# Kernel optimization log

Hardware: AMD Instinct MI355X
Metric: run time of the kernel (lower is better)

The kernel has to match this reference:

```python
import jax, jax.numpy as jnp
import numpy as np

DIM = 512
NUM_HEADS = 4  # min(4, 512 // 16)
HEAD_DIM = DIM // NUM_HEADS  # 128


def setup_inputs() -> dict:
    key = jax.random.key(0)
    ks = jax.random.split(key, 5)
    B, N = 2, 4096
    s = DIM ** -0.5
    return {
        "x": jax.random.normal(ks[0], (B, N, DIM), dtype=jnp.float32),
        "qkv_w": jax.random.normal(ks[1], (3 * DIM, DIM), dtype=jnp.float32) * s,
        "qkv_b": jax.random.normal(ks[2], (3 * DIM,), dtype=jnp.float32) * 0.02,
        "proj_w": jax.random.normal(ks[3], (DIM, DIM), dtype=jnp.float32) * s,
        "proj_b": jax.random.normal(ks[4], (DIM,), dtype=jnp.float32) * 0.02,
    }


def reference(x, qkv_w, qkv_b, proj_w, proj_b):
    B, N, C = x.shape
    H, D = NUM_HEADS, HEAD_DIM
    # torch Linear: x @ W^T + b
    qkv = x @ qkv_w.T + qkv_b                      # [B, N, 3C]
    qkv = qkv.reshape(B, N, 3, H, D)
    q = qkv[:, :, 0].transpose(0, 2, 1, 3)         # [B, H, N, D]
    k = qkv[:, :, 1].transpose(0, 2, 1, 3)
    v = qkv[:, :, 2].transpose(0, 2, 1, 3)
    scale = D ** -0.5
    attn = jnp.einsum('bhnd,bhmd->bhnm', q, k) * scale  # [B, H, N, N]
    attn = jax.nn.softmax(attn, axis=-1)
    # dropout(p=0.1) is identity in eval mode
    out = jnp.einsum('bhnm,bhmd->bhnd', attn, v)   # [B, H, N, D]
    out = out.transpose(0, 2, 1, 3).reshape(B, N, C)
    return out @ proj_w.T + proj_b
```

## Files before the change

### kernel.cpp

```cpp
#include <hip/hip_runtime.h>
#include <hip/hip_bf16.h>
#include <stdint.h>

constexpr int B_  = 2;
constexpr int N_  = 4096;
constexpr int C_  = 512;
constexpr int H_  = 4;
constexpr int D_  = 128;
constexpr int M_  = B_ * N_;
constexpr int TC_ = 3 * C_;
constexpr float SCALE_  = 0.08838834764831845f;
constexpr float LOG2E_  = 1.4426950408889634f;
constexpr float KSCALE_ = SCALE_ * LOG2E_;

typedef __attribute__((ext_vector_type(8))) short short8;
typedef __attribute__((ext_vector_type(4))) float f32x4;

#define GLOBAL_AS __attribute__((address_space(1)))
#define LDS_AS    __attribute__((address_space(3)))

static __device__ __forceinline__ void load_lds16(const void* gp, void* lp) {
    __builtin_amdgcn_global_load_lds((const GLOBAL_AS void*)gp, (LDS_AS void*)lp,
                                     16, 0, 0);
}

static __device__ __forceinline__ uint16_t f2bf(float f) {
    uint32_t u = __builtin_bit_cast(uint32_t, f);
    uint32_t r = (u + 0x7FFFu + ((u >> 16) & 1u)) >> 16;
    return (uint16_t)r;
}
static __device__ __forceinline__ uint32_t cvt_pk_bf16(float lo, float hi) {
    uint32_t r;
    asm("v_cvt_pk_bf16_f32 %0, %1, %2" : "=v"(r) : "v"(lo), "v"(hi));
    return r;
}
static __device__ __forceinline__ float exp2f_fast(float x) {
    float r;
    asm("v_exp_f32 %0, %1" : "=v"(r) : "v"(x));
    return r;
}

__global__ __launch_bounds__(256)
void cast_kernel(const float* __restrict__ src, uint16_t* __restrict__ dst, int n8)
{
    for (int i = blockIdx.x * blockDim.x + threadIdx.x; i < n8;
         i += gridDim.x * blockDim.x) {
        float4 a = reinterpret_cast<const float4*>(src)[2*i];
        float4 b = reinterpret_cast<const float4*>(src)[2*i+1];
        uint4 o;
        o.x = (uint32_t)f2bf(a.x) | ((uint32_t)f2bf(a.y) << 16);
        o.y = (uint32_t)f2bf(a.z) | ((uint32_t)f2bf(a.w) << 16);
        o.z = (uint32_t)f2bf(b.x) | ((uint32_t)f2bf(b.y) << 16);
        o.w = (uint32_t)f2bf(b.z) | ((uint32_t)f2bf(b.w) << 16);
        reinterpret_cast<uint4*>(dst)[i] = o;
    }
}

__global__ __launch_bounds__(256, 2)
void gemm_qkv(const uint16_t* __restrict__ A,
              const uint16_t* __restrict__ Bw,
              const float* __restrict__ bias,
              uint16_t* __restrict__ Qb,
              uint16_t* __restrict__ Kb,
              uint16_t* __restrict__ Vt)
{
    __shared__ __align__(16) uint16_t As[128 * 64];
    __shared__ __align__(16) uint16_t Bs[128 * 64];

    const int tid  = threadIdx.x;
    const int lane = tid & 63;
    const int w    = tid >> 6;
    const int wr   = w >> 1, wc = w & 1;
    const int cq   = lane & 15;
    const int g    = lane >> 4;
    const int m0   = blockIdx.x * 128;
    const int o0   = blockIdx.y * 128;

    f32x4 acc[4][4];
    const f32x4 zf = {0.f, 0.f, 0.f, 0.f};
    #pragma unroll
    for (int i = 0; i < 4; ++i)
        #pragma unroll
        for (int j = 0; j < 4; ++j) acc[i][j] = zf;

    for (int kt = 0; kt < C_; kt += 64) {
        __syncthreads();
        #pragma unroll
        for (int i = 0; i < 4; ++i) {
            int s = tid + 256 * i;
            int row = s >> 3, p = s & 7, c = p ^ (row & 7);
            load_lds16(A  + (size_t)(m0 + row) * C_ + kt + c * 8, &As[row*64 + p*8]);
            load_lds16(Bw + (size_t)(o0 + row) * C_ + kt + c * 8, &Bs[row*64 + p*8]);
        }
        __syncthreads();
        #pragma unroll
        for (int ks = 0; ks < 2; ++ks) {
            short8 af[4], bfr[4];
            #pragma unroll
            for (int mi = 0; mi < 4; ++mi) {
                int r = 64*wr + 16*mi + cq;
                af[mi] = *reinterpret_cast<const short8*>(
                    &As[r*64 + (((g + 4*ks) ^ (r & 7)) * 8)]);
            }
            #pragma unroll
            for (int ni = 0; ni < 4; ++ni) {
                int r = 64*wc + 16*ni + cq;
                bfr[ni] = *reinterpret_cast<const short8*>(
                    &Bs[r*64 + (((g + 4*ks) ^ (r & 7)) * 8)]);
            }
            #pragma unroll
            for (int mi = 0; mi < 4; ++mi)
                #pragma unroll
                for (int ni = 0; ni < 4; ++ni)
                    acc[mi][ni] = __builtin_amdgcn_mfma_f32_16x16x32_bf16(
                        af[mi], bfr[ni], acc[mi][ni], 0, 0, 0);
        }
    }

    const int sec = o0 >> 9;
    const int h   = (o0 >> 7) & 3;
    #pragma unroll
    for (int ni = 0; ni < 4; ++ni) {
        const int o = o0 + 64*wc + 16*ni + cq;
        const int d = o & 127;
        const float bv = bias[o];
        #pragma unroll
        for (int mi = 0; mi < 4; ++mi) {
            #pragma unroll
            for (int r = 0; r < 4; ++r) {
                const int m = m0 + 64*wr + 16*mi + 4*g + r;
                const int b = m >> 12;
                const int n = m & (N_ - 1);
                const float y = acc[mi][ni][r] + bv;
                if (sec == 0)
                    Qb[(((size_t)b*H_ + h)*N_ + n)*D_ + d] = f2bf(y);
                else if (sec == 1)
                    Kb[(((size_t)b*H_ + h)*N_ + n)*D_ + d] = f2bf(y * KSCALE_);
                else
                    Vt[(((size_t)b*H_ + h)*D_ + d)*N_ + n] = f2bf(y);
            }
        }
    }
}

__global__ __launch_bounds__(256, 1)
void attn_kernel(const uint16_t* __restrict__ Qb,
                 const uint16_t* __restrict__ Kb,
                 const uint16_t* __restrict__ Vt,
                 uint16_t* __restrict__ ctx)
{
    __shared__ __align__(16) uint16_t Ks[2][128 * 128];
    __shared__ __align__(16) uint16_t Vs[2][128 * 128];
    __shared__ __align__(16) uint16_t Ps[4][16 * 128];

    const int tid  = threadIdx.x;
    const int lane = tid & 63;
    const int w    = tid >> 6;
    const int cq   = lane & 15;
    const int g    = lane >> 4;

    const int bid = blockIdx.x;
    const int bh  = bid & 7;
    const int qt  = bid >> 3;
    const int b   = bh >> 2, h = bh & 3;

    const uint16_t* Qg = Qb + ((size_t)bh * N_ + qt * 128 + w * 32) * D_;
    const uint16_t* Kg = Kb + (size_t)bh * N_ * D_;
    const uint16_t* Vg = Vt + (size_t)bh * D_ * N_;

    auto stage = [&](int tn, int bb) {
        const int kv0 = tn * 128;
        #pragma unroll
        for (int i = 0; i < 8; ++i) {
            int s = tid + 256 * i;
            int row = s >> 4, p = s & 15, c = p ^ (row & 15);
            load_lds16(Kg + (size_t)(kv0 + row) * D_ + c * 8,
                       &Ks[bb][row * 128 + p * 8]);
        }
        #pragma unroll
        for (int i = 0; i < 8; ++i) {
            int s = tid + 256 * i;
            int row = s >> 4, p = s & 15, c = p ^ (row & 15);
            load_lds16(Vg + (size_t)row * N_ + kv0 + c * 8,
                       &Vs[bb][row * 128 + p * 8]);
        }
    };

    stage(0, 0);

    short8 qreg[2][4];
    #pragma unroll
    for (int qf = 0; qf < 2; ++qf) {
        const uint16_t* qrow = Qg + (size_t)(16 * qf + cq) * D_;
        #pragma unroll
        for (int ks = 0; ks < 4; ++ks)
            qreg[qf][ks] = *reinterpret_cast<const short8*>(qrow + 32*ks + 8*g);
    }

    float m_run[2] = {-3.0e38f, -3.0e38f};
    float l_run[2] = {0.f, 0.f};
    f32x4 o_acc[8][2];
    const f32x4 zf = {0.f, 0.f, 0.f, 0.f};
    #pragma unroll
    for (int df = 0; df < 8; ++df) { o_acc[df][0] = zf; o_acc[df][1] = zf; }

    __syncthreads();

    for (int t = 0; t < N_ / 128; ++t) {
        const int cur = t & 1;
        if (t + 1 < N_ / 128) stage(t + 1, cur ^ 1);

        f32x4 sacc[8][2];
        #pragma unroll
        for (int kvf = 0; kvf < 8; ++kvf) { sacc[kvf][0] = zf; sacc[kvf][1] = zf; }
        #pragma unroll
        for (int ks = 0; ks < 4; ++ks) {
            #pragma unroll
            for (int kvf = 0; kvf < 8; ++kvf) {
                const int row = 16 * kvf + cq;
                const short8 ak = *reinterpret_cast<const short8*>(
                    &Ks[cur][row * 128 + (((g + 4*ks) ^ cq) * 8)]);
                sacc[kvf][0] = __builtin_amdgcn_mfma_f32_16x16x32_bf16(
                    ak, qreg[0][ks], sacc[kvf][0], 0, 0, 0);
                sacc[kvf][1] = __builtin_amdgcn_mfma_f32_16x16x32_bf16(
                    ak, qreg[1][ks], sacc[kvf][1], 0, 0, 0);
            }
        }

        short8 bp[2][4];
        #pragma unroll
        for (int qf = 0; qf < 2; ++qf) {
            float pmax = -3.0e38f;
            #pragma unroll
            for (int kvf = 0; kvf < 8; ++kvf)
                #pragma unroll
                for (int r = 0; r < 4; ++r)
                    pmax = fmaxf(pmax, sacc[kvf][qf][r]);
            pmax = fmaxf(pmax, __shfl_xor(pmax, 16));
            pmax = fmaxf(pmax, __shfl_xor(pmax, 32));

            if (__any(pmax > m_run[qf] + 8.f)) {
                const float mnew = fmaxf(m_run[qf], pmax);
                const float corr = exp2f_fast(m_run[qf] - mnew);
                m_run[qf] = mnew;
                l_run[qf] *= corr;
                #pragma unroll
                for (int df = 0; df < 8; ++df)
                    #pragma unroll
                    for (int r = 0; r < 4; ++r)
                        o_acc[df][qf][r] *= corr;
            }

            float lsum = 0.f;
            #pragma unroll
            for (int kvf = 0; kvf < 8; ++kvf) {
                const float p0 = exp2f_fast(sacc[kvf][qf][0] - m_run[qf]);
                const float p1 = exp2f_fast(sacc[kvf][qf][1] - m_run[qf]);
                const float p2 = exp2f_fast(sacc[kvf][qf][2] - m_run[qf]);
                const float p3 = exp2f_fast(sacc[kvf][qf][3] - m_run[qf]);
                lsum += (p0 + p1) + (p2 + p3);
                const uint32_t w0 = cvt_pk_bf16(p0, p1);
                const uint32_t w1 = cvt_pk_bf16(p2, p3);
                const int cw = 2 * kvf + (g >> 1);
                *reinterpret_cast<uint2*>(
                    &Ps[w][cq * 128 + ((cw ^ cq) * 8 + 4 * (g & 1))]) =
                    make_uint2(w0, w1);
            }
            lsum += __shfl_xor(lsum, 16);
            lsum += __shfl_xor(lsum, 32);
            l_run[qf] += lsum;

            #pragma unroll
            for (int ks = 0; ks < 4; ++ks)
                bp[qf][ks] = *reinterpret_cast<const short8*>(
                    &Ps[w][cq * 128 + (((g + 4*ks) ^ cq) * 8)]);
        }

        #pragma unroll
        for (int ks = 0; ks < 4; ++ks) {
            #pragma unroll
            for (int df = 0; df < 8; ++df) {
                const int row = 16 * df + cq;
                const short8 av = *reinterpret_cast<const short8*>(
                    &Vs[cur][row * 128 + (((g + 4*ks) ^ cq) * 8)]);
                o_acc[df][0] = __builtin_amdgcn_mfma_f32_16x16x32_bf16(
                    av, bp[0][ks], o_acc[df][0], 0, 0, 0);
                o_acc[df][1] = __builtin_amdgcn_mfma_f32_16x16x32_bf16(
                    av, bp[1][ks], o_acc[df][1], 0, 0, 0);
            }
        }
        __syncthreads();
    }

    #pragma unroll
    for (int qf = 0; qf < 2; ++qf) {
        const float inv = 1.f / l_run[qf];
        const int n = qt * 128 + w * 32 + 16 * qf + cq;
        uint16_t* dst = ctx + ((size_t)b * N_ + n) * C_ + h * D_;
        #pragma unroll
        for (int df = 0; df < 8; ++df)
            #pragma unroll
            for (int r = 0; r < 4; ++r)
                dst[16 * df + 4 * g + r] = f2bf(o_acc[df][qf][r] * inv);
    }
}

__global__ __launch_bounds__(256, 2)
void gemm_proj(const uint16_t* __restrict__ A,
               const uint16_t* __restrict__ Bw,
               const float* __restrict__ bias,
               float* __restrict__ out)
{
    __shared__ __align__(16) uint16_t As[128 * 64];
    __shared__ __align__(16) uint16_t Bs[128 * 64];

    const int tid  = threadIdx.x;
    const int lane = tid & 63;
    const int w    = tid >> 6;
    const int wr   = w >> 1, wc = w & 1;
    const int cq   = lane & 15;
    const int g    = lane >> 4;
    const int m0   = blockIdx.x * 128;
    const int o0   = blockIdx.y * 128;

    f32x4 acc[4][4];
    const f32x4 zf = {0.f, 0.f, 0.f, 0.f};
    #pragma unroll
    for (int i = 0; i < 4; ++i)
        #pragma unroll
        for (int j = 0; j < 4; ++j) acc[i][j] = zf;

    for (int kt = 0; kt < C_; kt += 64) {
        __syncthreads();
        #pragma unroll
        for (int i = 0; i < 4; ++i) {
            int s = tid + 256 * i;
            int row = s >> 3, p = s & 7, c = p ^ (row & 7);
            load_lds16(A  + (size_t)(m0 + row) * C_ + kt + c * 8, &As[row*64 + p*8]);
            load_lds16(Bw + (size_t)(o0 + row) * C_ + kt + c * 8, &Bs[row*64 + p*8]);
        }
        __syncthreads();
        #pragma unroll
        for (int ks = 0; ks < 2; ++ks) {
            short8 af[4], bfr[4];
            #pragma unroll
            for (int mi = 0; mi < 4; ++mi) {
                int r = 64*wr + 16*mi + cq;
                af[mi] = *reinterpret_cast<const short8*>(
                    &As[r*64 + (((g + 4*ks) ^ (r & 7)) * 8)]);
            }
            #pragma unroll
            for (int ni = 0; ni < 4; ++ni) {
                int r = 64*wc + 16*ni + cq;
                bfr[ni] = *reinterpret_cast<const short8*>(
                    &Bs[r*64 + (((g + 4*ks) ^ (r & 7)) * 8)]);
            }
            #pragma unroll
            for (int mi = 0; mi < 4; ++mi)
                #pragma unroll
                for (int ni = 0; ni < 4; ++ni)
                    acc[mi][ni] = __builtin_amdgcn_mfma_f32_16x16x32_bf16(
                        af[mi], bfr[ni], acc[mi][ni], 0, 0, 0);
        }
    }

    #pragma unroll
    for (int ni = 0; ni < 4; ++ni) {
        const int o = o0 + 64*wc + 16*ni + cq;
        const float bv = bias[o];
        #pragma unroll
        for (int mi = 0; mi < 4; ++mi) {
            #pragma unroll
            for (int r = 0; r < 4; ++r) {
                const int m = m0 + 64*wr + 16*mi + 4*g + r;
                out[(size_t)m * C_ + o] = acc[mi][ni][r] + bv;
            }
        }
    }
}

extern "C" void kernel_launch(void* const* d_in, const int* in_sizes, int n_in,
                              void* d_out, int out_size, void* d_ws, size_t ws_size,
                              hipStream_t stream)
{
    const float* x      = (const float*)d_in[0];
    const float* qkv_w  = (const float*)d_in[1];
    const float* qkv_b  = (const float*)d_in[2];
    const float* proj_w = (const float*)d_in[3];
    const float* proj_b = (const float*)d_in[4];
    float* out = (float*)d_out;

    uint16_t* xb  = (uint16_t*)d_ws;
    uint16_t* wb  = xb  + (size_t)M_ * C_;
    uint16_t* pwb = wb  + (size_t)TC_ * C_;
    uint16_t* Qb  = pwb + (size_t)C_ * C_;
    uint16_t* Kb  = Qb  + (size_t)B_ * H_ * N_ * D_;
    uint16_t* Vt  = Kb  + (size_t)B_ * H_ * N_ * D_;
    uint16_t* ctx = Vt  + (size_t)B_ * H_ * N_ * D_;

    cast_kernel<<<1024, 256, 0, stream>>>(x,      xb,  M_*C_/8);
    cast_kernel<<< 384, 256, 0, stream>>>(qkv_w,  wb,  TC_*C_/8);
    cast_kernel<<< 128, 256, 0, stream>>>(proj_w, pwb, C_*C_/8);

    gemm_qkv<<<dim3(M_/128, TC_/128), 256, 0, stream>>>(xb, wb, qkv_b, Qb, Kb, Vt);
    attn_kernel<<<(N_/128) * (B_*H_), 256, 0, stream>>>(Qb, Kb, Vt, ctx);
    gemm_proj<<<dim3(M_/128, C_/128), 256, 0, stream>>>(ctx, pwb, proj_b, out);
}
```

Before: 230.0 us.

## Split attention KV tile across two wave groups, fuse casts, coalesce V-transpose stores

The attention kernel goes from 256 to 512 threads. Each group of four waves handles half of every 128-key tile, and the two partial softmax states (max, sum, output) are merged through LDS at the end. The intent is more waves per CU to hide latency, since the grid has only 256 blocks. The three cast launches become one kernel, and the V section of the QKV GEMM now transposes through LDS so it writes 16-byte coalesced rows instead of scattered 2-byte stores. The costs are an extra merge step, extra LDS traffic and a new P buffer layout with no swizzle, which may cause bank conflicts.

Result: faster. 196.0 us (-14.8%).

```diff
diff --git a/kernel.cpp b/kernel.cpp
--- a/kernel.cpp
+++ b/kernel.cpp
@@ -41,19 +41,24 @@
 }
 
 __global__ __launch_bounds__(256)
-void cast_kernel(const float* __restrict__ src, uint16_t* __restrict__ dst, int n8)
+void cast3_kernel(const float* __restrict__ x,  const float* __restrict__ w,
+                  const float* __restrict__ pw,
+                  uint16_t* __restrict__ xb, uint16_t* __restrict__ wb,
+                  uint16_t* __restrict__ pwb)
 {
-    for (int i = blockIdx.x * blockDim.x + threadIdx.x; i < n8;
-         i += gridDim.x * blockDim.x) {
-        float4 a = reinterpret_cast<const float4*>(src)[2*i];
-        float4 b = reinterpret_cast<const float4*>(src)[2*i+1];
-        uint4 o;
-        o.x = (uint32_t)f2bf(a.x) | ((uint32_t)f2bf(a.y) << 16);
-        o.y = (uint32_t)f2bf(a.z) | ((uint32_t)f2bf(a.w) << 16);
-        o.z = (uint32_t)f2bf(b.x) | ((uint32_t)f2bf(b.y) << 16);
-        o.w = (uint32_t)f2bf(b.z) | ((uint32_t)f2bf(b.w) << 16);
-        reinterpret_cast<uint4*>(dst)[i] = o;
-    }
+    const int bid = blockIdx.x;
+    const float* src; uint16_t* dst; int i;
+    if (bid < 2048)      { src = x;  dst = xb;  i = bid * 256 + threadIdx.x; }
+    else if (bid < 2432) { src = w;  dst = wb;  i = (bid - 2048) * 256 + threadIdx.x; }
+    else                 { src = pw; dst = pwb; i = (bid - 2432) * 256 + threadIdx.x; }
+    float4 a = reinterpret_cast<const float4*>(src)[2*i];
+    float4 b = reinterpret_cast<const float4*>(src)[2*i+1];
+    uint4 o;
+    o.x = (uint32_t)f2bf(a.x) | ((uint32_t)f2bf(a.y) << 16);
+    o.y = (uint32_t)f2bf(a.z) | ((uint32_t)f2bf(a.w) << 16);
+    o.z = (uint32_t)f2bf(b.x) | ((uint32_t)f2bf(b.y) << 16);
+    o.w = (uint32_t)f2bf(b.z) | ((uint32_t)f2bf(b.w) << 16);
+    reinterpret_cast<uint4*>(dst)[i] = o;
 }
 
 __global__ __launch_bounds__(256, 2)
@@ -64,8 +69,9 @@
               uint16_t* __restrict__ Kb,
               uint16_t* __restrict__ Vt)
 {
-    __shared__ __align__(16) uint16_t As[128 * 64];
-    __shared__ __align__(16) uint16_t Bs[128 * 64];
+    __shared__ __align__(16) uint16_t SMEM[128 * 128];
+    uint16_t* As = SMEM;
+    uint16_t* Bs = SMEM + 128 * 64;
 
     const int tid  = threadIdx.x;
     const int lane = tid & 63;
@@ -119,31 +125,59 @@
 
     const int sec = o0 >> 9;
     const int h   = (o0 >> 7) & 3;
-    #pragma unroll
-    for (int ni = 0; ni < 4; ++ni) {
-        const int o = o0 + 64*wc + 16*ni + cq;
-        const int d = o & 127;
-        const float bv = bias[o];
-        #pragma unroll
-        for (int mi = 0; mi < 4; ++mi) {
-            #pragma unroll
-            for (int r = 0; r < 4; ++r) {
-                const int m = m0 + 64*wr + 16*mi + 4*g + r;
-                const int b = m >> 12;
-                const int n = m & (N_ - 1);
-                const float y = acc[mi][ni][r] + bv;
-                if (sec == 0)
-                    Qb[(((size_t)b*H_ + h)*N_ + n)*D_ + d] = f2bf(y);
-                else if (sec == 1)
-                    Kb[(((size_t)b*H_ + h)*N_ + n)*D_ + d] = f2bf(y * KSCALE_);
-                else
-                    Vt[(((size_t)b*H_ + h)*D_ + d)*N_ + n] = f2bf(y);
-            }
-        }
-    }
-}
-
-__global__ __launch_bounds__(256, 1)
+    if (sec < 2) {
+        #pragma unroll
+        for (int ni = 0; ni < 4; ++ni) {
+            const int o = o0 + 64*wc + 16*ni + cq;
+            const int d = o & 127;
+            const float bv = bias[o];
+            #pragma unroll
+            for (int mi = 0; mi < 4; ++mi) {
+                #pragma unroll
+                for (int r = 0; r < 4; ++r) {
+                    const int m = m0 + 64*wr + 16*mi + 4*g + r;
+                    const int b = m >> 12;
+                    const int n = m & (N_ - 1);
+                    const float y = acc[mi][ni][r] + bv;
+                    if (sec == 0)
+                        Qb[(((size_t)b*H_ + h)*N_ + n)*D_ + d] = f2bf(y);
+                    else
+                        Kb[(((size_t)b*H_ + h)*N_ + n)*D_ + d] = f2bf(y * KSCALE_);
+                }
+            }
+        }
+    } else {
+        __syncthreads();
+        uint16_t* T = SMEM;
+        #pragma unroll
+        for (int ni = 0; ni < 4; ++ni) {
+            const int ol = 64*wc + 16*ni + cq;
+            const float bv = bias[o0 + ol];
+            #pragma unroll
+            for (int mi = 0; mi < 4; ++mi) {
+                const int ml = 64*wr + 16*mi + 4*g;
+                const uint32_t w0 = (uint32_t)f2bf(acc[mi][ni][0] + bv)
+                                  | ((uint32_t)f2bf(acc[mi][ni][1] + bv) << 16);
+                const uint32_t w1 = (uint32_t)f2bf(acc[mi][ni][2] + bv)
+                                  | ((uint32_t)f2bf(acc[mi][ni][3] + bv) << 16);
+                *reinterpret_cast<uint2*>(&T[ol*128 + ml]) = make_uint2(w0, w1);
+            }
+        }
+        __syncthreads();
+        const int b = m0 >> 12;
+        #pragma unroll
+        for (int i = 0; i < 8; ++i) {
+            int s = tid + 256 * i;
+            int ro = s >> 4, mc = s & 15;
+            int4 v = *reinterpret_cast<const int4*>(&T[ro*128 + mc*8]);
+            const int n = (m0 & (N_ - 1)) + mc*8;
+            *reinterpret_cast<int4*>(
+                &Vt[(((size_t)b*H_ + h)*D_ + ro)*N_ + n]) = v;
+        }
+    }
+}
+
+__global__ __launch_bounds__(512, 1)
 void attn_kernel(const uint16_t* __restrict__ Qb,
                  const uint16_t* __restrict__ Kb,
                  const uint16_t* __restrict__ Vt,
@@ -151,11 +185,13 @@
 {
     __shared__ __align__(16) uint16_t Ks[2][128 * 128];
     __shared__ __align__(16) uint16_t Vs[2][128 * 128];
-    __shared__ __align__(16) uint16_t Ps[4][16 * 128];
+    __shared__ __align__(16) uint16_t Ps[8][16 * 80];
 
     const int tid  = threadIdx.x;
     const int lane = tid & 63;
     const int w    = tid >> 6;
+    const int qb   = w & 3;
+    const int kvh  = w >> 2;
     const int cq   = lane & 15;
     const int g    = lane >> 4;
 
@@ -164,22 +200,22 @@
     const int qt  = bid >> 3;
     const int b   = bh >> 2, h = bh & 3;
 
-    const uint16_t* Qg = Qb + ((size_t)bh * N_ + qt * 128 + w * 32) * D_;
+    const uint16_t* Qg = Qb + ((size_t)bh * N_ + qt * 128 + qb * 32) * D_;
     const uint16_t* Kg = Kb + (size_t)bh * N_ * D_;
     const uint16_t* Vg = Vt + (size_t)bh * D_ * N_;
 
     auto stage = [&](int tn, int bb) {
         const int kv0 = tn * 128;
         #pragma unroll
-        for (int i = 0; i < 8; ++i) {
-            int s = tid + 256 * i;
+        for (int i = 0; i < 4; ++i) {
+            int s = tid + 512 * i;
             int row = s >> 4, p = s & 15, c = p ^ (row & 15);
             load_lds16(Kg + (size_t)(kv0 + row) * D_ + c * 8,
                        &Ks[bb][row * 128 + p * 8]);
         }
         #pragma unroll
-        for (int i = 0; i < 8; ++i) {
-            int s = tid + 256 * i;
+        for (int i = 0; i < 4; ++i) {
+            int s = tid + 512 * i;
             int row = s >> 4, p = s & 15, c = p ^ (row & 15);
             load_lds16(Vg + (size_t)row * N_ + kv0 + c * 8,
                        &Vs[bb][row * 128 + p * 8]);
@@ -210,16 +246,16 @@
         const int cur = t & 1;
         if (t + 1 < N_ / 128) stage(t + 1, cur ^ 1);
 
-        f32x4 sacc[8][2];
-        #pragma unroll
-        for (int kvf = 0; kvf < 8; ++kvf) { sacc[kvf][0] = zf; sacc[kvf][1] = zf; }
+        f32x4 sacc[4][2];
+        #pragma unroll
+        for (int kvf = 0; kvf < 4; ++kvf) { sacc[kvf][0] = zf; sacc[kvf][1] = zf; }
         #pragma unroll
         for (int ks = 0; ks < 4; ++ks) {
             #pragma unroll
-            for (int kvf = 0; kvf < 8; ++kvf) {
-                const int row = 16 * kvf + cq;
+            for (int kvf = 0; kvf < 4; ++kvf) {
+                const int row = kvh*64 + 16*kvf + cq;
                 const short8 ak = *reinterpret_cast<const short8*>(
-                    &Ks[cur][row * 128 + (((g + 4*ks) ^ cq) * 8)]);
+                    &Ks[cur][row * 128 + (((g + 4*ks) ^ (row & 15)) * 8)]);
                 sacc[kvf][0] = __builtin_amdgcn_mfma_f32_16x16x32_bf16(
                     ak, qreg[0][ks], sacc[kvf][0], 0, 0, 0);
                 sacc[kvf][1] = __builtin_amdgcn_mfma_f32_16x16x32_bf16(
@@ -227,12 +263,12 @@
             }
         }
 
-        short8 bp[2][4];
+        short8 bp[2][2];
         #pragma unroll
         for (int qf = 0; qf < 2; ++qf) {
             float pmax = -3.0e38f;
             #pragma unroll
-            for (int kvf = 0; kvf < 8; ++kvf)
+            for (int kvf = 0; kvf < 4; ++kvf)
                 #pragma unroll
                 for (int r = 0; r < 4; ++r)
                     pmax = fmaxf(pmax, sacc[kvf][qf][r]);
@@ -253,36 +289,33 @@
 
             float lsum = 0.f;
             #pragma unroll
-            for (int kvf = 0; kvf < 8; ++kvf) {
+            for (int kvf = 0; kvf < 4; ++kvf) {
                 const float p0 = exp2f_fast(sacc[kvf][qf][0] - m_run[qf]);
                 const float p1 = exp2f_fast(sacc[kvf][qf][1] - m_run[qf]);
                 const float p2 = exp2f_fast(sacc[kvf][qf][2] - m_run[qf]);
                 const float p3 = exp2f_fast(sacc[kvf][qf][3] - m_run[qf]);
                 lsum += (p0 + p1) + (p2 + p3);
-                const uint32_t w0 = cvt_pk_bf16(p0, p1);
-                const uint32_t w1 = cvt_pk_bf16(p2, p3);
-                const int cw = 2 * kvf + (g >> 1);
-                *reinterpret_cast<uint2*>(
-                    &Ps[w][cq * 128 + ((cw ^ cq) * 8 + 4 * (g & 1))]) =
-                    make_uint2(w0, w1);
+                *reinterpret_cast<uint2*>(&Ps[w][cq*80 + 16*kvf + 4*g]) =
+                    make_uint2(cvt_pk_bf16(p0, p1), cvt_pk_bf16(p2, p3));
             }
             lsum += __shfl_xor(lsum, 16);
             lsum += __shfl_xor(lsum, 32);
             l_run[qf] += lsum;
 
             #pragma unroll
-            for (int ks = 0; ks < 4; ++ks)
+            for (int ks = 0; ks < 2; ++ks)
                 bp[qf][ks] = *reinterpret_cast<const short8*>(
-                    &Ps[w][cq * 128 + (((g + 4*ks) ^ cq) * 8)]);
-        }
-
-        #pragma unroll
-        for (int ks = 0; ks < 4; ++ks) {
+                    &Ps[w][cq*80 + (4*ks + g) * 8]);
+        }
+
+        #pragma unroll
+        for (int ks = 0; ks < 2; ++ks) {
             #pragma unroll
             for (int df = 0; df < 8; ++df) {
-                const int row = 16 * df + cq;
+                const int row = 16*df + cq;
+                const int ch  = kvh*8 + 4*ks + g;
                 const short8 av = *reinterpret_cast<const short8*>(
-                    &Vs[cur][row * 128 + (((g + 4*ks) ^ cq) * 8)]);
+                    &Vs[cur][row * 128 + ((ch ^ (row & 15)) * 8)]);
                 o_acc[df][0] = __builtin_amdgcn_mfma_f32_16x16x32_bf16(
                     av, bp[0][ks], o_acc[df][0], 0, 0, 0);
                 o_acc[df][1] = __builtin_amdgcn_mfma_f32_16x16x32_bf16(
@@ -292,16 +325,47 @@
         __syncthreads();
     }
 
-    #pragma unroll
-    for (int qf = 0; qf < 2; ++qf) {
-        const float inv = 1.f / l_run[qf];
-        const int n = qt * 128 + w * 32 + 16 * qf + cq;
-        uint16_t* dst = ctx + ((size_t)b * N_ + n) * C_ + h * D_;
+    float* mbuf = reinterpret_cast<float*>(&Ks[0][0]);
+    float* lbuf = mbuf + 256;
+    f32x4* obuf = reinterpret_cast<f32x4*>(&Vs[0][0]);
+
+    if (kvh == 1) {
+        #pragma unroll
+        for (int qf = 0; qf < 2; ++qf) {
+            mbuf[(qb*2 + qf)*16 + cq] = m_run[qf];
+            lbuf[(qb*2 + qf)*16 + cq] = l_run[qf];
+        }
         #pragma unroll
         for (int df = 0; df < 8; ++df)
             #pragma unroll
-            for (int r = 0; r < 4; ++r)
-                dst[16 * df + 4 * g + r] = f2bf(o_acc[df][qf][r] * inv);
+            for (int qf = 0; qf < 2; ++qf)
+                obuf[qb*1024 + (df*2 + qf)*64 + lane] = o_acc[df][qf];
+    }
+    __syncthreads();
+    if (kvh == 0) {
+        #pragma unroll
+        for (int qf = 0; qf < 2; ++qf) {
+            const float mB = mbuf[(qb*2 + qf)*16 + cq];
+            const float lB = lbuf[(qb*2 + qf)*16 + cq];
+            const float ms = fmaxf(m_run[qf], mB);
+            const float cA = exp2f_fast(m_run[qf] - ms);
+            const float cB = exp2f_fast(mB - ms);
+            const float inv = 1.f / (l_run[qf] * cA + lB * cB);
+
+            const int n = qt*128 + qb*32 + 16*qf + cq;
+            uint16_t* dst = ctx + ((size_t)b * N_ + n) * C_ + h * D_;
+            #pragma unroll
+            for (int df = 0; df < 8; ++df) {
+                const f32x4 oB = obuf[qb*1024 + (df*2 + qf)*64 + lane];
+                float v0 = (o_acc[df][qf][0]*cA + oB[0]*cB) * inv;
+                float v1 = (o_acc[df][qf][1]*cA + oB[1]*cB) * inv;
+                float v2 = (o_acc[df][qf][2]*cA + oB[2]*cB) * inv;
+                float v3 = (o_acc[df][qf][3]*cA + oB[3]*cB) * inv;
+                const uint32_t w0 = (uint32_t)f2bf(v0) | ((uint32_t)f2bf(v1) << 16);
+                const uint32_t w1 = (uint32_t)f2bf(v2) | ((uint32_t)f2bf(v3) << 16);
+                *reinterpret_cast<uint2*>(&dst[16*df + 4*g]) = make_uint2(w0, w1);
+            }
+        }
     }
 }
 
@@ -398,11 +462,8 @@
     uint16_t* Vt  = Kb  + (size_t)B_ * H_ * N_ * D_;
     uint16_t* ctx = Vt  + (size_t)B_ * H_ * N_ * D_;
 
-    cast_kernel<<<1024, 256, 0, stream>>>(x,      xb,  M_*C_/8);
-    cast_kernel<<< 384, 256, 0, stream>>>(qkv_w,  wb,  TC_*C_/8);
-    cast_kernel<<< 128, 256, 0, stream>>>(proj_w, pwb, C_*C_/8);
-
+    cast3_kernel<<<2560, 256, 0, stream>>>(x, qkv_w, proj_w, xb, wb, pwb);
     gemm_qkv<<<dim3(M_/128, TC_/128), 256, 0, stream>>>(xb, wb, qkv_b, Qb, Kb, Vt);
-    attn_kernel<<<(N_/128) * (B_*H_), 256, 0, stream>>>(Qb, Kb, Vt, ctx);
+    attn_kernel<<<(N_/128) * (B_*H_), 512, 0, stream>>>(Qb, Kb, Vt, ctx);
     gemm_proj<<<dim3(M_/128, C_/128), 256, 0, stream>>>(ctx, pwb, proj_b, out);
 }
```
